# Kernel optimization log

Hardware: AMD Instinct MI355X
Metric: run time of the kernel (lower is better)

The kernel has to match this reference:

```python
import jax, jax.numpy as jnp
import numpy as np

RENORM_PERIOD = 256
MAX_NORM = 100.0


def setup_inputs() -> dict:
    key = jax.random.key(0)
    ks = jax.random.split(key, 9)
    B, S, G, D, N = 4, 2048, 8, 128, 64
    return {
        "x_r": jax.random.normal(ks[0], (B, S, G, D), jnp.float32),
        "x_i": jax.random.normal(ks[1], (B, S, G, D), jnp.float32),
        "log_A_mag": jax.random.uniform(ks[2], (G, N), jnp.float32) * 0.5 + 0.5,
        "A_phase": jax.random.normal(ks[3], (G, N), jnp.float32) * 0.1,
        "Bw_r": jax.random.normal(ks[4], (N, D), jnp.float32) / np.sqrt(D),
        "Bw_i": jax.random.normal(ks[5], (N, D), jnp.float32) / np.sqrt(D),
        "Cw_r": jax.random.normal(ks[6], (D, N), jnp.float32) / np.sqrt(N),
        "Cw_i": jax.random.normal(ks[7], (D, N), jnp.float32) / np.sqrt(N),
        "dt_w": jax.random.normal(ks[8], (2, 2 * D), jnp.float32) * 0.02,
        "dt_b": jnp.zeros((2,), jnp.float32),
    }


def reference(x_r, x_i, log_A_mag, A_phase, Bw_r, Bw_i, Cw_r, Cw_i, dt_w, dt_b):
    B, S, G, D = x_r.shape
    N = Bw_r.shape[0]
    # dt: input-dependent step magnitude / phase scale, clamped
    x_cat = jnp.concatenate([x_r, x_i], axis=-1)            # [B,S,G,2D]
    dt = jnp.clip(jnp.exp(jnp.einsum('bsgd,od->bsgo', x_cat, dt_w) + dt_b), 1e-4, 2.0)
    dt_mag = dt[..., 0:1]                                    # [B,S,G,1]
    dt_phase = dt[..., 1:2]
    # A_bar in polar form, |A| = exp(-softplus(log_A_mag)*dt_mag) < 1
    neg_log_A = -jax.nn.softplus(log_A_mag)[None, None]      # [1,1,G,N]
    A_mag = jnp.exp(dt_mag * neg_log_A)                      # [B,S,G,N]
    A_ang = dt_phase * A_phase[None, None]
    A_r = A_mag * jnp.cos(A_ang)
    A_i = A_mag * jnp.sin(A_ang)
    # Bx = (B_proj @ x) * dt_mag, complex linear
    Bx_r = (jnp.einsum('bsgd,nd->bsgn', x_r, Bw_r) - jnp.einsum('bsgd,nd->bsgn', x_i, Bw_i)) * dt_mag
    Bx_i = (jnp.einsum('bsgd,nd->bsgn', x_r, Bw_i) + jnp.einsum('bsgd,nd->bsgn', x_i, Bw_r)) * dt_mag

    def step(carry, inp):
        h_r, h_i = carry
        ar, ai, br, bi, t = inp
        nh_r = ar * h_r - ai * h_i + br
        nh_i = ar * h_i + ai * h_r + bi
        renorm = ((t + 1) % RENORM_PERIOD) == 0
        norm = jnp.sqrt(nh_r * nh_r + nh_i * nh_i + 1e-8)
        scale = jnp.minimum(norm, MAX_NORM) / norm
        nh_r = jnp.where(renorm, nh_r * scale, nh_r)
        nh_i = jnp.where(renorm, nh_i * scale, nh_i)
        return (nh_r, nh_i), (nh_r, nh_i)

    h0 = (jnp.zeros((B, G, N), jnp.float32), jnp.zeros((B, G, N), jnp.float32))
    xs = (jnp.moveaxis(A_r, 1, 0), jnp.moveaxis(A_i, 1, 0),
          jnp.moveaxis(Bx_r, 1, 0), jnp.moveaxis(Bx_i, 1, 0),
          jnp.arange(S))
    _, (all_h_r, all_h_i) = jax.lax.scan(step, h0, xs)       # [S,B,G,N]
    all_h_r = jnp.moveaxis(all_h_r, 0, 1)                    # [B,S,G,N]
    all_h_i = jnp.moveaxis(all_h_i, 0, 1)
    # y = C_proj(h), complex linear N -> D
    y_r = jnp.einsum('bsgn,dn->bsgd', all_h_r, Cw_r) - jnp.einsum('bsgn,dn->bsgd', all_h_i, Cw_i)
    y_i = jnp.einsum('bsgn,dn->bsgd', all_h_r, Cw_i) + jnp.einsum('bsgn,dn->bsgd', all_h_i, Cw_r)
    return jnp.stack([y_r, y_i], axis=0)                     # [2,B,S,G,D]
```

## Files before the change

### kernel.cpp

```cpp
#include <hip/hip_runtime.h>
#include <math.h>

#define B_ 4
#define S_ 2048
#define G_ 8
#define D_ 128
#define N_ 64
#define ROWS (B_*S_*G_)
#define CH 64
#define CLEN 32
#define NCHAIN (B_*G_*N_)
#define YOFF (ROWS*D_)

typedef short bf16x8 __attribute__((ext_vector_type(8)));
typedef float f32x4  __attribute__((ext_vector_type(4)));
#define MFMA16(a,b,c) __builtin_amdgcn_mfma_f32_16x16x32_bf16(a,b,c,0,0,0)

__device__ __forceinline__ unsigned short bf16_rtne(float f) {
    unsigned u = __float_as_uint(f);
    unsigned r = (u + 0x7FFFu + ((u >> 16) & 1u)) >> 16;
    return (unsigned short)r;
}
__device__ __forceinline__ void split_bf16(float f, unsigned short &hi, unsigned short &lo) {
    hi = bf16_rtne(f);
    float hif = __uint_as_float(((unsigned)hi) << 16);
    lo = bf16_rtne(f - hif);
}
__device__ __forceinline__ void split4(float4 v, uint2 &hi2, uint2 &lo2) {
    unsigned short h0,h1,h2,h3,l0,l1,l2,l3;
    split_bf16(v.x,h0,l0); split_bf16(v.y,h1,l1);
    split_bf16(v.z,h2,l2); split_bf16(v.w,h3,l3);
    hi2 = make_uint2((unsigned)h0 | ((unsigned)h1<<16), (unsigned)h2 | ((unsigned)h3<<16));
    lo2 = make_uint2((unsigned)l0 | ((unsigned)l1<<16), (unsigned)l2 | ((unsigned)l3<<16));
}
__device__ __forceinline__ float dot4(float4 a, float4 b) {
    return fmaf(a.x,b.x, fmaf(a.y,b.y, fmaf(a.z,b.z, a.w*b.w)));
}

__global__ __launch_bounds__(256) void k_prep(
    const float* __restrict__ bwr, const float* __restrict__ bwi,
    const float* __restrict__ cwr, const float* __restrict__ cwi,
    unsigned short* __restrict__ wbhi, unsigned short* __restrict__ wblo,
    unsigned short* __restrict__ wchi)
{
    int tid = blockIdx.x * 256 + threadIdx.x;
    if (tid < 4096) {
        int f = tid;
        int lane = f & 63, ks = (f >> 6) & 7, nt = (f >> 9) & 1, w = f >> 10;
        int l15 = lane & 15, quad = lane >> 4;
        int n = w * 32 + nt * 16 + l15;
        int k0 = ks * 32 + quad * 8;
        const float* src; float sgn = 1.f;
        if (n < 64) {
            if (k0 < 128) src = bwr + n * 128 + k0;
            else        { src = bwi + n * 128 + (k0 - 128); sgn = -1.f; }
        } else {
            if (k0 < 128) src = bwi + (n - 64) * 128 + k0;
            else          src = bwr + (n - 64) * 128 + (k0 - 128);
        }
        float4 v0 = *(const float4*)src;
        float4 v1 = *(const float4*)(src + 4);
        float vv[8] = {v0.x,v0.y,v0.z,v0.w,v1.x,v1.y,v1.z,v1.w};
        unsigned short h[8], l[8];
        #pragma unroll
        for (int j = 0; j < 8; j++) split_bf16(vv[j] * sgn, h[j], l[j]);
        #pragma unroll
        for (int j = 0; j < 8; j++) { wbhi[f*8+j] = h[j]; wblo[f*8+j] = l[j]; }
    } else {
        int f = tid - 4096;
        int lane = f & 63, ks = (f >> 6) & 3, nt = (f >> 8) & 3, w = f >> 10;
        int l15 = lane & 15, quad = lane >> 4;
        int n = w * 64 + nt * 16 + l15;
        int d = (n < 128) ? n : (n - 128);
        int k0 = ks * 32 + quad * 8;
        const float* src; float sgn = 1.f;
        if (n < 128) {
            if (k0 < 64) src = cwr + d * 64 + k0;
            else       { src = cwi + d * 64 + (k0 - 64); sgn = -1.f; }
        } else {
            if (k0 < 64) src = cwi + d * 64 + k0;
            else         src = cwr + d * 64 + (k0 - 64);
        }
        float4 v0 = *(const float4*)src;
        float4 v1 = *(const float4*)(src + 4);
        float vv[8] = {v0.x,v0.y,v0.z,v0.w,v1.x,v1.y,v1.z,v1.w};
        unsigned short h[8], l[8];
        #pragma unroll
        for (int j = 0; j < 8; j++) split_bf16(vv[j] * sgn, h[j], l[j]);
        #pragma unroll
        for (int j = 0; j < 8; j++) wchi[f*8+j] = h[j];
    }
}

#define LDK1 280
__global__ __launch_bounds__(256, 2) void k_g1(
    const float* __restrict__ xr, const float* __restrict__ xi,
    const float* __restrict__ dtw, const float* __restrict__ dtb,
    const float* __restrict__ logAm, const float* __restrict__ Aph,
    const unsigned short* __restrict__ wbhi, const unsigned short* __restrict__ wblo,
    float* __restrict__ bxr, float* __restrict__ bxi,
    float* __restrict__ dt_mag, float* __restrict__ dt_ph,
    float4* __restrict__ trans)
{
    __shared__ __align__(16) unsigned short Ahi[32 * LDK1];
    __shared__ __align__(16) unsigned short Alo[32 * LDK1];
    __shared__ float dms[32], dps[32];
    __shared__ float4 comb[64];
    float* bxs = (float*)Ahi;
    const int t = threadIdx.x;
    const int lane = t & 63, w = t >> 6;
    const int l15 = lane & 15, quad = lane >> 4;
    const int bg = blockIdx.x >> 4, cq = blockIdx.x & 15;
    const int g = bg & 7, b = bg >> 3;

    bf16x8 wh[2][8], wl[2][8];
    #pragma unroll
    for (int nt = 0; nt < 2; nt++)
        #pragma unroll
        for (int ks = 0; ks < 8; ks++) {
            int idx = ((w * 2 + nt) * 8 + ks) * 64 + lane;
            wh[nt][ks] = ((const bf16x8*)wbhi)[idx];
            wl[nt][ks] = ((const bf16x8*)wblo)[idx];
        }

    const int kq = t & 31, k4 = kq * 4;
    float4 w0r = *(const float4*)(dtw + k4);
    float4 w0i = *(const float4*)(dtw + 128 + k4);
    float4 w1r = *(const float4*)(dtw + 256 + k4);
    float4 w1i = *(const float4*)(dtw + 384 + k4);
    float b0 = dtb[0], b1 = dtb[1];
    float nla = -logf(1.0f + __expf(logAm[g * N_ + lane]));
    float aph = Aph[g * N_ + lane];

    for (int it = 0; it < 4; it++) {
        __syncthreads();
        const int c  = cq * 4 + it;
        const int s0 = c * CLEN;
        const float* xrb = xr + ((size_t)(b * S_ + s0) * G_ + g) * 128;
        const float* xib = xi + ((size_t)(b * S_ + s0) * G_ + g) * 128;
        float pm[4], pp[4];
        #pragma unroll
        for (int i = 0; i < 4; i++) {
            int f = t + 256 * i;
            int m = f >> 5, kk = f & 31;
            float4 a  = ((const float4*)(xrb + m * 1024))[kk];
            float4 bb = ((const float4*)(xib + m * 1024))[kk];
            uint2 h2, l2;
            split4(a, h2, l2);
            *(uint2*)&Ahi[m * LDK1 + kk * 4] = h2;
            *(uint2*)&Alo[m * LDK1 + kk * 4] = l2;
            split4(bb, h2, l2);
            *(uint2*)&Ahi[m * LDK1 + 128 + kk * 4] = h2;
            *(uint2*)&Alo[m * LDK1 + 128 + kk * 4] = l2;
            pm[i] = dot4(a, w0r) + dot4(bb, w0i);
            pp[i] = dot4(a, w1r) + dot4(bb, w1i);
        }
        #pragma unroll
        for (int i = 0; i < 4; i++) {
            float vm = pm[i], vp = pp[i];
            #pragma unroll
            for (int msk = 16; msk >= 1; msk >>= 1) {
                vm += __shfl_xor(vm, msk);
                vp += __shfl_xor(vp, msk);
            }
            if ((t & 31) == 0) {
                int m = (t >> 5) + 8 * i;
                float dm = fminf(fmaxf(__expf(vm + b0), 1e-4f), 2.0f);
                float dp = fminf(fmaxf(__expf(vp + b1), 1e-4f), 2.0f);
                dms[m] = dm; dps[m] = dp;
                int row = (b * S_ + s0 + m) * G_ + g;
                dt_mag[row] = dm; dt_ph[row] = dp;
            }
        }
        __syncthreads();

        f32x4 acc[2][2];
        #pragma unroll
        for (int a = 0; a < 2; a++)
            #pragma unroll
            for (int bq = 0; bq < 2; bq++)
                acc[a][bq] = (f32x4){0.f, 0.f, 0.f, 0.f};
        #pragma unroll
        for (int ms = 0; ms < 2; ms++) {
            int arow = (ms * 16 + l15) * LDK1 + quad * 8;
            #pragma unroll
            for (int ks = 0; ks < 8; ks++) {
                bf16x8 ah = *(const bf16x8*)&Ahi[arow + ks * 32];
                bf16x8 al = *(const bf16x8*)&Alo[arow + ks * 32];
                #pragma unroll
                for (int nt = 0; nt < 2; nt++) {
                    acc[ms][nt] = MFMA16(al, wh[nt][ks], acc[ms][nt]);
                    acc[ms][nt] = MFMA16(ah, wl[nt][ks], acc[ms][nt]);
                    acc[ms][nt] = MFMA16(ah, wh[nt][ks], acc[ms][nt]);
                }
            }
        }
        __syncthreads();

        #pragma unroll
        for (int ms = 0; ms < 2; ms++)
            #pragma unroll
            for (int nt = 0; nt < 2; nt++) {
                int n = w * 32 + nt * 16 + l15;
                float* dstg = (n < 64) ? bxr : bxi;
                int nn = n & 63;
                #pragma unroll
                for (int r = 0; r < 4; r++) {
                    int m = ms * 16 + quad * 4 + r;
                    float v = acc[ms][nt][r] * dms[m];
                    dstg[((b * S_ + s0 + m) * G_ + g) * 64 + nn] = v;
                    bxs[m * 132 + n] = v;
                }
            }
        __syncthreads();

        float Ar = 1.f, Ai = 0.f, Br = 0.f, Bi = 0.f;
        if (w < 2) {
            int base = w * 16;
            #pragma unroll
            for (int tt = 0; tt < 16; tt++) {
                int m = base + tt;
                float dm = dms[m], dp = dps[m];
                float am  = __expf(dm * nla);
                float ang = dp * aph;
                float cr = am * __cosf(ang), ci = am * __sinf(ang);
                float vr = bxs[m * 132 + lane], vi = bxs[m * 132 + 64 + lane];
                float nAr = cr * Ar - ci * Ai;
                float nAi = cr * Ai + ci * Ar;
                float nBr = cr * Br - ci * Bi + vr;
                float nBi = cr * Bi + ci * Br + vi;
                Ar = nAr; Ai = nAi; Br = nBr; Bi = nBi;
            }
            if (w == 0) comb[lane] = make_float4(Ar, Ai, Br, Bi);
        }
        __syncthreads();
        if (w == 1) {
            float4 c0 = comb[lane];
            float fAr = Ar * c0.x - Ai * c0.y;
            float fAi = Ar * c0.y + Ai * c0.x;
            float fBr = Ar * c0.z - Ai * c0.w + Br;
            float fBi = Ar * c0.w + Ai * c0.z + Bi;
            trans[(bg * CH + c) * 64 + lane] = make_float4(fAr, fAi, fBr, fBi);
        }
    }
}

__global__ __launch_bounds__(256) void k_scanB2(const float4* __restrict__ trans,
    float2* __restrict__ hstart)
{
    int w = threadIdx.x >> 6, lane = threadIdx.x & 63;
    int W = blockIdx.x * 4 + w;
    int bg = W >> 3;
    int n  = ((W & 7) << 3) + (lane & 7);
    int j  = lane >> 3;
    float pAr[8], pAi[8], pBr[8], pBi[8];
    float Ar = 1.f, Ai = 0.f, Br = 0.f, Bi = 0.f;
    const float4* tp = trans + (bg * CH + j * 8) * 64 + n;
    #pragma unroll
    for (int k = 0; k < 8; k++) {
        pAr[k] = Ar; pAi[k] = Ai; pBr[k] = Br; pBi[k] = Bi;
        float4 T = tp[k * 64];
        float nAr = T.x * Ar - T.y * Ai;
        float nAi = T.x * Ai + T.y * Ar;
        float nBr = T.x * Br - T.y * Bi + T.z;
        float nBi = T.x * Bi + T.y * Br + T.w;
        Ar = nAr; Ai = nAi; Br = nBr; Bi = nBi;
    }
    float hr = 0.f, hi = 0.f, mhr = 0.f, mhi = 0.f;
    #pragma unroll
    for (int j2 = 0; j2 < 8; j2++) {
        if (j2 == j) { mhr = hr; mhi = hi; }
        int src = j2 * 8 + (lane & 7);
        float sAr = __shfl(Ar, src), sAi = __shfl(Ai, src);
        float sBr = __shfl(Br, src), sBi = __shfl(Bi, src);
        float nr = sAr * hr - sAi * hi + sBr;
        float ni = sAr * hi + sAi * hr + sBi;
        float nrm = sqrtf(nr * nr + ni * ni + 1e-8f);
        float sc = fminf(nrm, 100.f) / nrm;
        hr = nr * sc; hi = ni * sc;
    }
    float2* hp = hstart + (bg * CH + j * 8) * 64 + n;
    #pragma unroll
    for (int k = 0; k < 8; k++) {
        float hsr = pAr[k] * mhr - pAi[k] * mhi + pBr[k];
        float hsi = pAr[k] * mhi + pAi[k] * mhr + pBi[k];
        hp[k * 64] = make_float2(hsr, hsi);
    }
}

#define LDK2 152
__global__ __launch_bounds__(256, 2) void k_sg2(
    const float* __restrict__ bxr, const float* __restrict__ bxi,
    const float* __restrict__ dt_mag, const float* __restrict__ dt_ph,
    const float* __restrict__ logAm, const float* __restrict__ Aph,
    const float2* __restrict__ hstart,
    const unsigned short* __restrict__ wchi,
    float* __restrict__ out)
{
    __shared__ __align__(16) unsigned short Ahi[128 * LDK2];
    __shared__ __align__(16) unsigned short Alo[128 * LDK2];
    const int t = threadIdx.x;
    const int lane = t & 63, w = t >> 6;
    const int l15 = lane & 15, quad = lane >> 4;
    const int bg = blockIdx.x >> 4, cq = blockIdx.x & 15;
    const int g = bg & 7, b = bg >> 3;

    bf16x8 wc[4][4];
    #pragma unroll
    for (int nt = 0; nt < 4; nt++)
        #pragma unroll
        for (int ks = 0; ks < 4; ks++)
            wc[nt][ks] = ((const bf16x8*)wchi)[((w * 4 + nt) * 4 + ks) * 64 + lane];

    {
        const int n = lane;
        const int c = cq * 4 + w;
        float nla = -logf(1.0f + __expf(logAm[g * N_ + n]));
        float aph = Aph[g * N_ + n];
        float2 h0 = hstart[(bg * CH + c) * 64 + n];
        float hr = h0.x, hi = h0.y;
        const bool rn = ((c & 7) == 7);
        const int rowbase = (b * S_ + c * CLEN) * G_ + g;
        #pragma unroll 8
        for (int tt = 0; tt < CLEN; tt++) {
            int row = rowbase + tt * G_;
            float dm = dt_mag[row], dp = dt_ph[row];
            float am  = __expf(dm * nla);
            float ang = dp * aph;
            float cr = am * __cosf(ang), ci = am * __sinf(ang);
            float vr = bxr[row * N_ + n], vi = bxi[row * N_ + n];
            float nr = cr * hr - ci * hi + vr;
            float ni = cr * hi + ci * hr + vi;
            if (rn && tt == CLEN - 1) {
                float nrm = sqrtf(nr * nr + ni * ni + 1e-8f);
                float scale = fminf(nrm, 100.0f) / nrm;
                nr *= scale; ni *= scale;
            }
            hr = nr; hi = ni;
            int m = w * 32 + tt;
            unsigned short hh, hl;
            split_bf16(hr, hh, hl);
            Ahi[m * LDK2 + n] = hh;  Alo[m * LDK2 + n] = hl;
            split_bf16(hi, hh, hl);
            Ahi[m * LDK2 + 64 + n] = hh;  Alo[m * LDK2 + 64 + n] = hl;
        }
    }
    __syncthreads();

    #pragma unroll
    for (int mh = 0; mh < 2; mh++) {
        f32x4 acc[4][4];
        #pragma unroll
        for (int a = 0; a < 4; a++)
            #pragma unroll
            for (int bq = 0; bq < 4; bq++)
                acc[a][bq] = (f32x4){0.f, 0.f, 0.f, 0.f};
        #pragma unroll
        for (int ms = 0; ms < 4; ms++) {
            int arow = (mh * 64 + ms * 16 + l15) * LDK2 + quad * 8;
            #pragma unroll
            for (int ks = 0; ks < 4; ks++) {
                bf16x8 ah = *(const bf16x8*)&Ahi[arow + ks * 32];
                bf16x8 al = *(const bf16x8*)&Alo[arow + ks * 32];
                #pragma unroll
                for (int nt = 0; nt < 4; nt++) {
                    acc[ms][nt] = MFMA16(al, wc[nt][ks], acc[ms][nt]);
                    acc[ms][nt] = MFMA16(ah, wc[nt][ks], acc[ms][nt]);
                }
            }
        }
        #pragma unroll
        for (int ms = 0; ms < 4; ms++)
            #pragma unroll
            for (int nt = 0; nt < 4; nt++) {
                int nn = w * 64 + nt * 16 + l15;
                float* dst = (nn < 128) ? (out + nn) : (out + YOFF + (nn - 128));
                #pragma unroll
                for (int r = 0; r < 4; r++) {
                    int m_local = mh * 64 + ms * 16 + quad * 4 + r;
                    int cc = m_local >> 5, tt2 = m_local & 31;
                    int srow = (b * S_ + (cq * 4 + cc) * CLEN + tt2) * G_ + g;
                    dst[srow * 128] = acc[ms][nt][r];
                }
            }
    }
}

extern "C" void kernel_launch(void* const* d_in, const int* in_sizes, int n_in,
                              void* d_out, int out_size, void* d_ws, size_t ws_size,
                              hipStream_t stream) {
    (void)in_sizes; (void)n_in; (void)out_size; (void)ws_size;
    const float* xr    = (const float*)d_in[0];
    const float* xi    = (const float*)d_in[1];
    const float* logAm = (const float*)d_in[2];
    const float* Aph   = (const float*)d_in[3];
    const float* bwr   = (const float*)d_in[4];
    const float* bwi   = (const float*)d_in[5];
    const float* cwr   = (const float*)d_in[6];
    const float* cwi   = (const float*)d_in[7];
    const float* dtw   = (const float*)d_in[8];
    const float* dtb   = (const float*)d_in[9];
    float* out = (float*)d_out;
    float* ws  = (float*)d_ws;

    float*  dt_mag = ws;
    float*  dt_ph  = ws + 65536;
    float*  bxr    = ws + 131072;
    float*  bxi    = bxr + 4194304;
    float4* trans  = (float4*)(ws + 8519680);
    float2* hstart = (float2*)(ws + 9043968);
    unsigned short* wbhi = (unsigned short*)(ws + 9306112);
    unsigned short* wblo = wbhi + 32768;
    unsigned short* wchi = wblo + 32768;

    hipLaunchKernelGGL(k_prep,   dim3(32), dim3(256), 0, stream,
                       bwr, bwi, cwr, cwi, wbhi, wblo, wchi);
    hipLaunchKernelGGL(k_g1,     dim3((B_ * G_) * 16), dim3(256), 0, stream,
                       xr, xi, dtw, dtb, logAm, Aph, wbhi, wblo,
                       bxr, bxi, dt_mag, dt_ph, trans);
    hipLaunchKernelGGL(k_scanB2, dim3(64), dim3(256), 0, stream,
                       trans, hstart);
    hipLaunchKernelGGL(k_sg2,    dim3((B_ * G_) * 16), dim3(256), 0, stream,
                       bxr, bxi, dt_mag, dt_ph, logAm, Aph, hstart, wchi, out);
}
```

Measured before the change: 163.7 us.

## Drop split-bf16 precision, pack Bx as bf16 pairs, fold chunk scan into consumer

Several changes at once. The weight lo-part and the hi/lo split of activations are removed, so the GEMMs run fewer MFMAs in plain bf16. Bx is stored as packed bf16 real/imag pairs to halve that intermediate's traffic. The separate inter-chunk scan kernel is removed, and each k_sg2 wave instead recomputes its start state by walking the chunk transitions serially. k_g1 is split into twice as many blocks with a higher occupancy hint. This trades accuracy and some redundant serial work in k_sg2 for less memory traffic, fewer MFMAs and one fewer launch.

```diff
diff --git a/kernel.cpp b/kernel.cpp
--- a/kernel.cpp
+++ b/kernel.cpp
@@ -9,7 +9,6 @@
 #define ROWS (B_*S_*G_)
 #define CH 64
 #define CLEN 32
-#define NCHAIN (B_*G_*N_)
 #define YOFF (ROWS*D_)
 
 typedef short bf16x8 __attribute__((ext_vector_type(8)));
@@ -40,8 +39,7 @@
 __global__ __launch_bounds__(256) void k_prep(
     const float* __restrict__ bwr, const float* __restrict__ bwi,
     const float* __restrict__ cwr, const float* __restrict__ cwi,
-    unsigned short* __restrict__ wbhi, unsigned short* __restrict__ wblo,
-    unsigned short* __restrict__ wchi)
+    unsigned short* __restrict__ wbhi, unsigned short* __restrict__ wchi)
 {
     int tid = blockIdx.x * 256 + threadIdx.x;
     if (tid < 4096) {
@@ -61,11 +59,8 @@
         float4 v0 = *(const float4*)src;
         float4 v1 = *(const float4*)(src + 4);
         float vv[8] = {v0.x,v0.y,v0.z,v0.w,v1.x,v1.y,v1.z,v1.w};
-        unsigned short h[8], l[8];
-        #pragma unroll
-        for (int j = 0; j < 8; j++) split_bf16(vv[j] * sgn, h[j], l[j]);
-        #pragma unroll
-        for (int j = 0; j < 8; j++) { wbhi[f*8+j] = h[j]; wblo[f*8+j] = l[j]; }
+        #pragma unroll
+        for (int j = 0; j < 8; j++) wbhi[f*8+j] = bf16_rtne(vv[j] * sgn);
     } else {
         int f = tid - 4096;
         int lane = f & 63, ks = (f >> 6) & 3, nt = (f >> 8) & 3, w = f >> 10;
@@ -84,21 +79,18 @@
         float4 v0 = *(const float4*)src;
         float4 v1 = *(const float4*)(src + 4);
         float vv[8] = {v0.x,v0.y,v0.z,v0.w,v1.x,v1.y,v1.z,v1.w};
-        unsigned short h[8], l[8];
-        #pragma unroll
-        for (int j = 0; j < 8; j++) split_bf16(vv[j] * sgn, h[j], l[j]);
-        #pragma unroll
-        for (int j = 0; j < 8; j++) wchi[f*8+j] = h[j];
+        #pragma unroll
+        for (int j = 0; j < 8; j++) wchi[f*8+j] = bf16_rtne(vv[j] * sgn);
     }
 }
 
 #define LDK1 280
-__global__ __launch_bounds__(256, 2) void k_g1(
+__global__ __launch_bounds__(256, 4) void k_g1(
     const float* __restrict__ xr, const float* __restrict__ xi,
     const float* __restrict__ dtw, const float* __restrict__ dtb,
     const float* __restrict__ logAm, const float* __restrict__ Aph,
-    const unsigned short* __restrict__ wbhi, const unsigned short* __restrict__ wblo,
-    float* __restrict__ bxr, float* __restrict__ bxi,
+    const unsigned short* __restrict__ wbhi,
+    unsigned int* __restrict__ bxp,
     float* __restrict__ dt_mag, float* __restrict__ dt_ph,
     float4* __restrict__ trans)
 {
@@ -110,18 +102,15 @@
     const int t = threadIdx.x;
     const int lane = t & 63, w = t >> 6;
     const int l15 = lane & 15, quad = lane >> 4;
-    const int bg = blockIdx.x >> 4, cq = blockIdx.x & 15;
+    const int bg = blockIdx.x >> 5, cq = blockIdx.x & 31;
     const int g = bg & 7, b = bg >> 3;
 
-    bf16x8 wh[2][8], wl[2][8];
+    bf16x8 wh[2][8];
     #pragma unroll
     for (int nt = 0; nt < 2; nt++)
         #pragma unroll
-        for (int ks = 0; ks < 8; ks++) {
-            int idx = ((w * 2 + nt) * 8 + ks) * 64 + lane;
-            wh[nt][ks] = ((const bf16x8*)wbhi)[idx];
-            wl[nt][ks] = ((const bf16x8*)wblo)[idx];
-        }
+        for (int ks = 0; ks < 8; ks++)
+            wh[nt][ks] = ((const bf16x8*)wbhi)[((w * 2 + nt) * 8 + ks) * 64 + lane];
 
     const int kq = t & 31, k4 = kq * 4;
     float4 w0r = *(const float4*)(dtw + k4);
@@ -132,9 +121,9 @@
     float nla = -logf(1.0f + __expf(logAm[g * N_ + lane]));
     float aph = Aph[g * N_ + lane];
 
-    for (int it = 0; it < 4; it++) {
-        __syncthreads();
-        const int c  = cq * 4 + it;
+    for (int it = 0; it < 2; it++) {
+        __syncthreads();
+        const int c  = cq * 2 + it;
         const int s0 = c * CLEN;
         const float* xrb = xr + ((size_t)(b * S_ + s0) * G_ + g) * 128;
         const float* xib = xi + ((size_t)(b * S_ + s0) * G_ + g) * 128;
@@ -190,7 +179,6 @@
                 #pragma unroll
                 for (int nt = 0; nt < 2; nt++) {
                     acc[ms][nt] = MFMA16(al, wh[nt][ks], acc[ms][nt]);
-                    acc[ms][nt] = MFMA16(ah, wl[nt][ks], acc[ms][nt]);
                     acc[ms][nt] = MFMA16(ah, wh[nt][ks], acc[ms][nt]);
                 }
             }
@@ -202,17 +190,22 @@
             #pragma unroll
             for (int nt = 0; nt < 2; nt++) {
                 int n = w * 32 + nt * 16 + l15;
-                float* dstg = (n < 64) ? bxr : bxi;
-                int nn = n & 63;
                 #pragma unroll
                 for (int r = 0; r < 4; r++) {
                     int m = ms * 16 + quad * 4 + r;
-                    float v = acc[ms][nt][r] * dms[m];
-                    dstg[((b * S_ + s0 + m) * G_ + g) * 64 + nn] = v;
-                    bxs[m * 132 + n] = v;
+                    bxs[m * 132 + n] = acc[ms][nt][r] * dms[m];
                 }
             }
         __syncthreads();
+
+        #pragma unroll
+        for (int j = 0; j < 8; j++) {
+            int idx = j * 256 + t;
+            int m = idx >> 6, n = idx & 63;
+            float vr = bxs[m * 132 + n], vi = bxs[m * 132 + 64 + n];
+            unsigned pr = bf16_rtne(vr), pi = bf16_rtne(vi);
+            bxp[((b * S_ + s0 + m) * G_ + g) * 64 + n] = pr | (pi << 16);
+        }
 
         float Ar = 1.f, Ai = 0.f, Br = 0.f, Bi = 0.f;
         if (w < 2) {
@@ -245,60 +238,16 @@
     }
 }
 
-__global__ __launch_bounds__(256) void k_scanB2(const float4* __restrict__ trans,
-    float2* __restrict__ hstart)
-{
-    int w = threadIdx.x >> 6, lane = threadIdx.x & 63;
-    int W = blockIdx.x * 4 + w;
-    int bg = W >> 3;
-    int n  = ((W & 7) << 3) + (lane & 7);
-    int j  = lane >> 3;
-    float pAr[8], pAi[8], pBr[8], pBi[8];
-    float Ar = 1.f, Ai = 0.f, Br = 0.f, Bi = 0.f;
-    const float4* tp = trans + (bg * CH + j * 8) * 64 + n;
-    #pragma unroll
-    for (int k = 0; k < 8; k++) {
-        pAr[k] = Ar; pAi[k] = Ai; pBr[k] = Br; pBi[k] = Bi;
-        float4 T = tp[k * 64];
-        float nAr = T.x * Ar - T.y * Ai;
-        float nAi = T.x * Ai + T.y * Ar;
-        float nBr = T.x * Br - T.y * Bi + T.z;
-        float nBi = T.x * Bi + T.y * Br + T.w;
-        Ar = nAr; Ai = nAi; Br = nBr; Bi = nBi;
-    }
-    float hr = 0.f, hi = 0.f, mhr = 0.f, mhi = 0.f;
-    #pragma unroll
-    for (int j2 = 0; j2 < 8; j2++) {
-        if (j2 == j) { mhr = hr; mhi = hi; }
-        int src = j2 * 8 + (lane & 7);
-        float sAr = __shfl(Ar, src), sAi = __shfl(Ai, src);
-        float sBr = __shfl(Br, src), sBi = __shfl(Bi, src);
-        float nr = sAr * hr - sAi * hi + sBr;
-        float ni = sAr * hi + sAi * hr + sBi;
-        float nrm = sqrtf(nr * nr + ni * ni + 1e-8f);
-        float sc = fminf(nrm, 100.f) / nrm;
-        hr = nr * sc; hi = ni * sc;
-    }
-    float2* hp = hstart + (bg * CH + j * 8) * 64 + n;
-    #pragma unroll
-    for (int k = 0; k < 8; k++) {
-        float hsr = pAr[k] * mhr - pAi[k] * mhi + pBr[k];
-        float hsi = pAr[k] * mhi + pAi[k] * mhr + pBi[k];
-        hp[k * 64] = make_float2(hsr, hsi);
-    }
-}
-
-#define LDK2 152
-__global__ __launch_bounds__(256, 2) void k_sg2(
-    const float* __restrict__ bxr, const float* __restrict__ bxi,
+#define LDK2 136
+__global__ __launch_bounds__(256, 4) void k_sg2(
+    const unsigned int* __restrict__ bxp,
     const float* __restrict__ dt_mag, const float* __restrict__ dt_ph,
     const float* __restrict__ logAm, const float* __restrict__ Aph,
-    const float2* __restrict__ hstart,
+    const float4* __restrict__ trans,
     const unsigned short* __restrict__ wchi,
     float* __restrict__ out)
 {
     __shared__ __align__(16) unsigned short Ahi[128 * LDK2];
-    __shared__ __align__(16) unsigned short Alo[128 * LDK2];
     const int t = threadIdx.x;
     const int lane = t & 63, w = t >> 6;
     const int l15 = lane & 15, quad = lane >> 4;
@@ -315,10 +264,21 @@
     {
         const int n = lane;
         const int c = cq * 4 + w;
+        float hr = 0.f, hi = 0.f;
+        const float4* tp = trans + (bg * CH) * 64 + n;
+        for (int k = 0; k < c; k++) {
+            float4 T = tp[k * 64];
+            float nr = T.x * hr - T.y * hi + T.z;
+            float ni = T.x * hi + T.y * hr + T.w;
+            if ((k & 7) == 7) {
+                float nrm = sqrtf(nr * nr + ni * ni + 1e-8f);
+                float sc = fminf(nrm, 100.f) / nrm;
+                nr *= sc; ni *= sc;
+            }
+            hr = nr; hi = ni;
+        }
         float nla = -logf(1.0f + __expf(logAm[g * N_ + n]));
         float aph = Aph[g * N_ + n];
-        float2 h0 = hstart[(bg * CH + c) * 64 + n];
-        float hr = h0.x, hi = h0.y;
         const bool rn = ((c & 7) == 7);
         const int rowbase = (b * S_ + c * CLEN) * G_ + g;
         #pragma unroll 8
@@ -328,7 +288,9 @@
             float am  = __expf(dm * nla);
             float ang = dp * aph;
             float cr = am * __cosf(ang), ci = am * __sinf(ang);
-            float vr = bxr[row * N_ + n], vi = bxi[row * N_ + n];
+            unsigned p = bxp[row * 64 + n];
+            float vr = __uint_as_float(p << 16);
+            float vi = __uint_as_float(p & 0xFFFF0000u);
             float nr = cr * hr - ci * hi + vr;
             float ni = cr * hi + ci * hr + vi;
             if (rn && tt == CLEN - 1) {
@@ -338,51 +300,37 @@
             }
             hr = nr; hi = ni;
             int m = w * 32 + tt;
-            unsigned short hh, hl;
-            split_bf16(hr, hh, hl);
-            Ahi[m * LDK2 + n] = hh;  Alo[m * LDK2 + n] = hl;
-            split_bf16(hi, hh, hl);
-            Ahi[m * LDK2 + 64 + n] = hh;  Alo[m * LDK2 + 64 + n] = hl;
+            Ahi[m * LDK2 + n]      = bf16_rtne(hr);
+            Ahi[m * LDK2 + 64 + n] = bf16_rtne(hi);
         }
     }
     __syncthreads();
 
     #pragma unroll
-    for (int mh = 0; mh < 2; mh++) {
-        f32x4 acc[4][4];
-        #pragma unroll
-        for (int a = 0; a < 4; a++)
-            #pragma unroll
-            for (int bq = 0; bq < 4; bq++)
-                acc[a][bq] = (f32x4){0.f, 0.f, 0.f, 0.f};
-        #pragma unroll
-        for (int ms = 0; ms < 4; ms++) {
-            int arow = (mh * 64 + ms * 16 + l15) * LDK2 + quad * 8;
-            #pragma unroll
-            for (int ks = 0; ks < 4; ks++) {
-                bf16x8 ah = *(const bf16x8*)&Ahi[arow + ks * 32];
-                bf16x8 al = *(const bf16x8*)&Alo[arow + ks * 32];
-                #pragma unroll
-                for (int nt = 0; nt < 4; nt++) {
-                    acc[ms][nt] = MFMA16(al, wc[nt][ks], acc[ms][nt]);
-                    acc[ms][nt] = MFMA16(ah, wc[nt][ks], acc[ms][nt]);
-                }
-            }
-        }
-        #pragma unroll
-        for (int ms = 0; ms < 4; ms++)
-            #pragma unroll
-            for (int nt = 0; nt < 4; nt++) {
-                int nn = w * 64 + nt * 16 + l15;
-                float* dst = (nn < 128) ? (out + nn) : (out + YOFF + (nn - 128));
-                #pragma unroll
-                for (int r = 0; r < 4; r++) {
-                    int m_local = mh * 64 + ms * 16 + quad * 4 + r;
-                    int cc = m_local >> 5, tt2 = m_local & 31;
-                    int srow = (b * S_ + (cq * 4 + cc) * CLEN + tt2) * G_ + g;
-                    dst[srow * 128] = acc[ms][nt][r];
-                }
-            }
+    for (int ms = 0; ms < 8; ms++) {
+        f32x4 acc[4];
+        #pragma unroll
+        for (int nt = 0; nt < 4; nt++) acc[nt] = (f32x4){0.f, 0.f, 0.f, 0.f};
+        int arow = (ms * 16 + l15) * LDK2 + quad * 8;
+        #pragma unroll
+        for (int ks = 0; ks < 4; ks++) {
+            bf16x8 ah = *(const bf16x8*)&Ahi[arow + ks * 32];
+            #pragma unroll
+            for (int nt = 0; nt < 4; nt++)
+                acc[nt] = MFMA16(ah, wc[nt][ks], acc[nt]);
+        }
+        #pragma unroll
+        for (int nt = 0; nt < 4; nt++) {
+            int nn = w * 64 + nt * 16 + l15;
+            float* dst = (nn < 128) ? (out + nn) : (out + YOFF + (nn - 128));
+            #pragma unroll
+            for (int r = 0; r < 4; r++) {
+                int m_local = ms * 16 + quad * 4 + r;
+                int cc = m_local >> 5, tt2 = m_local & 31;
+                int srow = (b * S_ + (cq * 4 + cc) * CLEN + tt2) * G_ + g;
+                dst[srow * 128] = acc[nt][r];
+            }
+        }
     }
 }
 
@@ -403,23 +351,18 @@
     float* out = (float*)d_out;
     float* ws  = (float*)d_ws;
 
-    float*  dt_mag = ws;
-    float*  dt_ph  = ws + 65536;
-    float*  bxr    = ws + 131072;
-    float*  bxi    = bxr + 4194304;
-    float4* trans  = (float4*)(ws + 8519680);
-    float2* hstart = (float2*)(ws + 9043968);
-    unsigned short* wbhi = (unsigned short*)(ws + 9306112);
-    unsigned short* wblo = wbhi + 32768;
-    unsigned short* wchi = wblo + 32768;
-
-    hipLaunchKernelGGL(k_prep,   dim3(32), dim3(256), 0, stream,
-                       bwr, bwi, cwr, cwi, wbhi, wblo, wchi);
-    hipLaunchKernelGGL(k_g1,     dim3((B_ * G_) * 16), dim3(256), 0, stream,
-                       xr, xi, dtw, dtb, logAm, Aph, wbhi, wblo,
-                       bxr, bxi, dt_mag, dt_ph, trans);
-    hipLaunchKernelGGL(k_scanB2, dim3(64), dim3(256), 0, stream,
-                       trans, hstart);
-    hipLaunchKernelGGL(k_sg2,    dim3((B_ * G_) * 16), dim3(256), 0, stream,
-                       bxr, bxi, dt_mag, dt_ph, logAm, Aph, hstart, wchi, out);
-}
+    float*        dt_mag = ws;
+    float*        dt_ph  = ws + 65536;
+    unsigned int* bxp    = (unsigned int*)(ws + 131072);
+    float4*       trans  = (float4*)(ws + 4325376);
+    unsigned short* wbhi = (unsigned short*)(ws + 4849664);
+    unsigned short* wchi = wbhi + 32768;
+
+    hipLaunchKernelGGL(k_prep, dim3(32), dim3(256), 0, stream,
+                       bwr, bwi, cwr, cwi, wbhi, wchi);
+    hipLaunchKernelGGL(k_g1,   dim3((B_ * G_) * 32), dim3(256), 0, stream,
+                       xr, xi, dtw, dtb, logAm, Aph, wbhi,
+                       bxp, dt_mag, dt_ph, trans);
+    hipLaunchKernelGGL(k_sg2,  dim3((B_ * G_) * 16), dim3(256), 0, stream,
+                       bxp, dt_mag, dt_ph, logAm, Aph, trans, wchi, out);
+}
```

New measurement: 216.6 us. 32.3% more time.
